# Optimization experiments

Hardware: AMD Instinct MI355X
Metric: run time of the kernel (lower is better)

Reference implementation:

```python
import jax, jax.numpy as jnp
import numpy as np

NUM_EXPERTS = 8
TOP_K = 2
HIDDEN = 2048
INTER = 7168
B, S = 4, 2048


def setup_inputs() -> dict:
    key = jax.random.key(0)
    k0, k1, k2, k3, k4 = jax.random.split(key, 5)
    scale_h = 1.0 / np.sqrt(HIDDEN)
    scale_i = 1.0 / np.sqrt(INTER)
    return {
        "hidden_states": jax.random.normal(k0, (B, S, HIDDEN), dtype=jnp.float32),
        "gate_w": jax.random.normal(k1, (NUM_EXPERTS, HIDDEN), dtype=jnp.float32) * scale_h,
        "w1": jax.random.normal(k2, (NUM_EXPERTS, INTER, HIDDEN), dtype=jnp.float32) * scale_h,
        "w3": jax.random.normal(k3, (NUM_EXPERTS, INTER, HIDDEN), dtype=jnp.float32) * scale_h,
        "w2": jax.random.normal(k4, (NUM_EXPERTS, HIDDEN, INTER), dtype=jnp.float32) * scale_i,
    }


def reference(hidden_states, gate_w, w1, w3, w2):
    orig_shape = hidden_states.shape
    x = hidden_states.reshape(-1, HIDDEN)              # [T, H]

    # Router: gate linear -> softmax -> top-k -> renormalize.
    router_logits = x @ gate_w.T                       # [T, E]
    probs = jax.nn.softmax(router_logits, axis=-1)
    topk_w, topk_idx = jax.lax.top_k(probs, TOP_K)     # [T, K]
    topk_w = topk_w / jnp.sum(topk_w, axis=-1, keepdims=True)

    # Dense combine weights: [T, E] with top-k renormalized weights scattered.
    combine = jnp.sum(
        jax.nn.one_hot(topk_idx, NUM_EXPERTS, dtype=x.dtype) * topk_w[..., None],
        axis=1,
    )                                                   # [T, E]

    out = jnp.zeros_like(x)
    # Fixed small loop over experts (structurally distinct weight matrices);
    # avoids materializing a [T, E, I] intermediate.
    for e in range(NUM_EXPERTS):
        g = jax.nn.silu(x @ w1[e].T)                   # [T, I]
        u = x @ w3[e].T                                # [T, I]
        y = (g * u) @ w2[e].T                          # [T, H]
        out = out + combine[:, e:e + 1] * y

    return out.reshape(orig_shape)
```

## Files before the change

kernel.cpp:

```cpp
#include <hip/hip_runtime.h>
#include <stdint.h>

#define NE    8
#define HID   2048
#define INTER 7168
#define TTOK  8192
#define NT1   (HID / 64)
#define NT2   (INTER / 64)

typedef __bf16 bf16;
typedef bf16 bf16x4 __attribute__((ext_vector_type(4)));
typedef bf16 bf16x8 __attribute__((ext_vector_type(8)));
typedef float f32x4 __attribute__((ext_vector_type(4)));

__device__ __forceinline__ void glds16(const void* g, void* l) {
  __builtin_amdgcn_global_load_lds((__attribute__((address_space(1))) void*)g,
                                   (__attribute__((address_space(3))) void*)l, 16, 0, 0);
}

__global__ void cvt_f32_bf16(const float* __restrict__ src, bf16* __restrict__ dst, long n) {
  long i = (long)blockIdx.x * blockDim.x + threadIdx.x;
  long stride = (long)gridDim.x * blockDim.x;
  for (long j = i * 4; j < n; j += stride * 4) {
    float4 v = *(const float4*)(src + j);
    bf16x4 o = {(bf16)v.x, (bf16)v.y, (bf16)v.z, (bf16)v.w};
    *(bf16x4*)(dst + j) = o;
  }
}

__global__ void router_kernel(const float* __restrict__ x, const float* __restrict__ gw,
                              int* __restrict__ topk_e, float* __restrict__ topk_w) {
  const int wid = threadIdx.x >> 6, lane = threadIdx.x & 63;
  const int t = blockIdx.x * 4 + wid;
  if (t >= TTOK) return;
  const float* xr = x + (size_t)t * HID;
  float xv[32];
#pragma unroll
  for (int i = 0; i < 32; ++i) xv[i] = xr[lane + 64 * i];
  float lg[NE];
#pragma unroll
  for (int e = 0; e < NE; ++e) {
    const float* g = gw + e * HID;
    float s = 0.f;
#pragma unroll
    for (int i = 0; i < 32; ++i) s += xv[i] * g[lane + 64 * i];
#pragma unroll
    for (int off = 32; off; off >>= 1) s += __shfl_down(s, off);
    lg[e] = s;
  }
  if (lane == 0) {
    int i1 = 0;
#pragma unroll
    for (int e = 1; e < NE; ++e) if (lg[e] > lg[i1]) i1 = e;
    int i2 = (i1 == 0) ? 1 : 0;
#pragma unroll
    for (int e = 0; e < NE; ++e) if (e != i2 && e != i1 && lg[e] > lg[i2]) i2 = e;
    float r = __expf(lg[i2] - lg[i1]);
    float wa = 1.f / (1.f + r);
    topk_e[2 * t] = i1; topk_e[2 * t + 1] = i2;
    topk_w[2 * t] = wa; topk_w[2 * t + 1] = 1.f - wa;
  }
}

__global__ void gather_sorted(const int* __restrict__ topk_e, const float* __restrict__ topk_w,
                              int* __restrict__ cnt, int* __restrict__ ltok, float* __restrict__ lw) {
  const int e = blockIdx.x;
  const int tid = threadIdx.x;
  __shared__ int scan[256];
  __shared__ int basesh;
  if (tid == 0) basesh = 0;
  __syncthreads();
  for (int c0 = 0; c0 < TTOK; c0 += 256) {
    const int t = c0 + tid;
    const int e0 = topk_e[2 * t], e1 = topk_e[2 * t + 1];
    const int flag = (e0 == e) || (e1 == e);
    const float w = (e0 == e) ? topk_w[2 * t] : topk_w[2 * t + 1];
    scan[tid] = flag;
    __syncthreads();
    for (int off = 1; off < 256; off <<= 1) {
      int add = (tid >= off) ? scan[tid - off] : 0;
      __syncthreads();
      scan[tid] += add;
      __syncthreads();
    }
    const int rank = scan[tid] - flag;
    const int total = scan[255];
    const int base = basesh;
    if (flag) { ltok[e * TTOK + base + rank] = t; lw[e * TTOK + base + rank] = w; }
    __syncthreads();
    if (tid == 0) basesh = base + total;
    __syncthreads();
  }
  if (tid == 0) cnt[e] = basesh;
}

__global__ void prefix_kernel(const int* __restrict__ cnt, int* __restrict__ base) {
  if (threadIdx.x == 0 && blockIdx.x == 0) {
    int b = 0;
    for (int e = 0; e < NE; ++e) { base[e] = b; b += cnt[e]; }
  }
}


#define MFMA(a, b, c) __builtin_amdgcn_mfma_f32_16x16x32_bf16((a), (b), (c), 0, 0, 0)

#define STAGE_A(h, kt) do { int _b = ((kt) & 1) * 32768; size_t _k = (size_t)(kt) * 128; \
    glds16(bA + oA[(h)*2 + 0] + _k, ldsA + _b + (h) * 16384 + d0); \
    glds16(bA + oA[(h)*2 + 1] + _k, ldsA + _b + (h) * 16384 + d1); } while (0)
#define STAGE_B(h, kt) do { int _b = ((kt) & 1) * 32768; size_t _k = (size_t)(kt) * 128; \
    glds16(bB + oB[(h)*2 + 0] + _k, ldsB + _b + (h) * 16384 + d0); \
    glds16(bB + oB[(h)*2 + 1] + _k, ldsB + _b + (h) * 16384 + d1); } while (0)

#define RD_A(mf, ks) (*(const bf16x8*)(ldsA + curb + arow + (mf) * (16 * 128) + ((ks) ? kcol1 : kcol0)))
#define RD_B(nf, ks) (*(const bf16x8*)(ldsB + curb + brow + (nf) * (16 * 128) + ((ks) ? kcol1 : kcol0)))

#define BAR()   __builtin_amdgcn_s_barrier()
#define LGKM0() do { asm volatile("s_waitcnt lgkmcnt(0)" ::: "memory"); \
                     __builtin_amdgcn_sched_barrier(0); } while (0)
#define SCHED0() __builtin_amdgcn_sched_barrier(0)

__launch_bounds__(512, 2)
__global__ void pass1_kernel(const bf16* __restrict__ xb, const bf16* __restrict__ w1b,
                             bf16* __restrict__ hbuf, const int* __restrict__ cnt,
                             const int* __restrict__ basep, const int* __restrict__ ltok) {
  const int e = blockIdx.z;
  const int c = cnt[e];
  const int tm = blockIdx.y;
  if (tm * 256 >= c) return;
  const int tn = blockIdx.x;

  __shared__ __align__(16) bf16 sA[2][256 * 64];
  __shared__ __align__(16) bf16 sB[2][256 * 64];
  char* const ldsA = (char*)&sA[0][0];
  char* const ldsB = (char*)&sB[0][0];

  const int tid = threadIdx.x;
  const int r0 = tid >> 3;
  const int ls = (tid & 7) ^ (r0 & 7);
  const int d0 = tid * 16, d1 = (tid + 512) * 16;
  const char* const bA = (const char*)xb;
  const char* const bB = (const char*)w1b;

  uint32_t oA[4], oB[4];
#pragma unroll
  for (int i = 0; i < 4; ++i) {
    int trow = i * 64 + r0;
    int slot = tm * 256 + trow; if (slot >= c) slot = c - 1;
    oA[i] = (uint32_t)((size_t)ltok[e * TTOK + slot] * (HID * 2) + ls * 16);
    int br = i * 64 + r0;
    int w = (br >> 4) & 1;
    int wr = tn * 128 + ((br >> 5) << 4) + (br & 15);
    size_t off = ((size_t)e * INTER + wr) * (HID * 2) + (size_t)ls * 16;
    if (w) off += (size_t)NE * INTER * HID * 2;
    oB[i] = (uint32_t)off;
  }

  const int lane = tid & 63, wid = tid >> 6;
  const int wm = wid >> 2, wn = wid & 3;
  const int ln15 = lane & 15, kq = lane >> 4;
  const int swz = (ln15 & 7) << 4;
  const int kcol0 = (kq * 16) ^ swz;
  const int kcol1 = (64 + kq * 16) ^ swz;
  const int arow = (wm * 128 + ln15) * 128;
  const int brow = (wn * 64 + ln15) * 128;

  f32x4 acc[8][4];
#pragma unroll
  for (int m = 0; m < 8; ++m)
#pragma unroll
    for (int n = 0; n < 4; ++n) acc[m][n] = (f32x4){0.f, 0.f, 0.f, 0.f};

  STAGE_A(0, 0); STAGE_A(1, 0); STAGE_B(0, 0); STAGE_B(1, 0);
  asm volatile("s_waitcnt vmcnt(4)" ::: "memory");
  STAGE_A(0, 1); STAGE_A(1, 1); STAGE_B(0, 1);
  asm volatile("s_waitcnt vmcnt(6)" ::: "memory");
  BAR();

  bf16x8 a0[4][2], a1[4][2], b0[2][2], b1[2][2];
  int cur = 0;
  for (int t = 0; t < NT1; ++t, cur ^= 1) {
    const int curb = cur * 32768;
#pragma unroll
    for (int m = 0; m < 4; ++m) { a0[m][0] = RD_A(m, 0); a0[m][1] = RD_A(m, 1); }
#pragma unroll
    for (int n = 0; n < 2; ++n) { b0[n][0] = RD_B(n, 0); b0[n][1] = RD_B(n, 1); }
    if (t + 1 < NT1) STAGE_B(1, t + 1);
    BAR(); LGKM0();
    __builtin_amdgcn_s_setprio(1);
#pragma unroll
    for (int m = 0; m < 4; ++m)
#pragma unroll
      for (int n = 0; n < 2; ++n) {
        acc[m][n] = MFMA(a0[m][0], b0[n][0], acc[m][n]);
        acc[m][n] = MFMA(a0[m][1], b0[n][1], acc[m][n]);
      }
    __builtin_amdgcn_s_setprio(0);
    BAR();
#pragma unroll
    for (int m = 0; m < 4; ++m) { a1[m][0] = RD_A(4 + m, 0); a1[m][1] = RD_A(4 + m, 1); }
    BAR(); LGKM0();
    __builtin_amdgcn_s_setprio(1);
#pragma unroll
    for (int m = 0; m < 4; ++m)
#pragma unroll
      for (int n = 0; n < 2; ++n) {
        acc[4 + m][n] = MFMA(a1[m][0], b0[n][0], acc[4 + m][n]);
        acc[4 + m][n] = MFMA(a1[m][1], b0[n][1], acc[4 + m][n]);
      }
    __builtin_amdgcn_s_setprio(0);
    BAR();
#pragma unroll
    for (int n = 0; n < 2; ++n) { b1[n][0] = RD_B(2 + n, 0); b1[n][1] = RD_B(2 + n, 1); }
    if (t + 2 < NT1) { STAGE_A(0, t + 2); STAGE_A(1, t + 2); SCHED0(); }
    BAR(); LGKM0();
    __builtin_amdgcn_s_setprio(1);
#pragma unroll
    for (int m = 0; m < 4; ++m)
#pragma unroll
      for (int n = 0; n < 2; ++n) {
        acc[m][2 + n] = MFMA(a0[m][0], b1[n][0], acc[m][2 + n]);
        acc[m][2 + n] = MFMA(a0[m][1], b1[n][1], acc[m][2 + n]);
      }
    __builtin_amdgcn_s_setprio(0);
    BAR();
    if (t + 2 < NT1) STAGE_B(0, t + 2);
    __builtin_amdgcn_s_setprio(1);
#pragma unroll
    for (int m = 0; m < 4; ++m)
#pragma unroll
      for (int n = 0; n < 2; ++n) {
        acc[4 + m][2 + n] = MFMA(a1[m][0], b1[n][0], acc[4 + m][2 + n]);
        acc[4 + m][2 + n] = MFMA(a1[m][1], b1[n][1], acc[4 + m][2 + n]);
      }
    __builtin_amdgcn_s_setprio(0);
    if (t + 2 < NT1) asm volatile("s_waitcnt vmcnt(6)" ::: "memory");
    else             asm volatile("s_waitcnt vmcnt(0)" ::: "memory");
    BAR();
  }

  const int be = basep[e];
#pragma unroll
  for (int mh = 0; mh < 2; ++mh)
#pragma unroll
    for (int mf = 0; mf < 4; ++mf)
#pragma unroll
      for (int j = 0; j < 4; ++j) {
        const int slot = tm * 256 + wm * 128 + mh * 64 + mf * 16 + kq * 4 + j;
        if (slot < c) {
          bf16* hrow = hbuf + (size_t)(be + slot) * INTER + tn * 128;
#pragma unroll
          for (int p = 0; p < 2; ++p) {
            const float g = acc[mh * 4 + mf][2 * p][j];
            const float u = acc[mh * 4 + mf][2 * p + 1][j];
            const float hv = g / (1.f + __expf(-g)) * u;
            hrow[wn * 32 + p * 16 + ln15] = (bf16)hv;
          }
        }
      }
}

__launch_bounds__(512, 2)
__global__ void pass2_kernel(const bf16* __restrict__ hbuf, const bf16* __restrict__ w2b,
                             float* __restrict__ out, const int* __restrict__ cnt,
                             const int* __restrict__ basep, const int* __restrict__ ltok,
                             const float* __restrict__ lw) {
  const int e = blockIdx.z;
  const int c = cnt[e];
  const int tm = blockIdx.y;
  if (tm * 256 >= c) return;
  const int tn = blockIdx.x;

  __shared__ __align__(16) bf16 sA[2][256 * 64];
  __shared__ __align__(16) bf16 sB[2][256 * 64];
  char* const ldsA = (char*)&sA[0][0];
  char* const ldsB = (char*)&sB[0][0];

  const int tid = threadIdx.x;
  const int r0 = tid >> 3;
  const int ls = (tid & 7) ^ (r0 & 7);
  const int d0 = tid * 16, d1 = (tid + 512) * 16;
  const int be = basep[e];
  const char* const bA = (const char*)hbuf;
  const char* const bB = (const char*)w2b;

  uint32_t oA[4], oB[4];
#pragma unroll
  for (int i = 0; i < 4; ++i) {
    int trow = i * 64 + r0;
    int slot = tm * 256 + trow; if (slot >= c) slot = c - 1;
    oA[i] = (uint32_t)((size_t)(be + slot) * (INTER * 2) + ls * 16);
    oB[i] = (uint32_t)(((size_t)e * HID + tn * 256 + i * 64 + r0) * (INTER * 2) + (size_t)ls * 16);
  }

  const int lane = tid & 63, wid = tid >> 6;
  const int wm = wid >> 2, wn = wid & 3;
  const int ln15 = lane & 15, kq = lane >> 4;
  const int swz = (ln15 & 7) << 4;
  const int kcol0 = (kq * 16) ^ swz;
  const int kcol1 = (64 + kq * 16) ^ swz;
  const int arow = (wm * 128 + ln15) * 128;
  const int brow = (wn * 64 + ln15) * 128;

  f32x4 acc[8][4];
#pragma unroll
  for (int m = 0; m < 8; ++m)
#pragma unroll
    for (int n = 0; n < 4; ++n) acc[m][n] = (f32x4){0.f, 0.f, 0.f, 0.f};

  STAGE_A(0, 0); STAGE_A(1, 0); STAGE_B(0, 0); STAGE_B(1, 0);
  asm volatile("s_waitcnt vmcnt(4)" ::: "memory");
  STAGE_A(0, 1); STAGE_A(1, 1); STAGE_B(0, 1);
  asm volatile("s_waitcnt vmcnt(6)" ::: "memory");
  BAR();

  bf16x8 a0[4][2], a1[4][2], b0[2][2], b1[2][2];
  int cur = 0;
  for (int t = 0; t < NT2; ++t, cur ^= 1) {
    const int curb = cur * 32768;
#pragma unroll
    for (int m = 0; m < 4; ++m) { a0[m][0] = RD_A(m, 0); a0[m][1] = RD_A(m, 1); }
#pragma unroll
    for (int n = 0; n < 2; ++n) { b0[n][0] = RD_B(n, 0); b0[n][1] = RD_B(n, 1); }
    if (t + 1 < NT2) STAGE_B(1, t + 1);
    BAR(); LGKM0();
    __builtin_amdgcn_s_setprio(1);
#pragma unroll
    for (int m = 0; m < 4; ++m)
#pragma unroll
      for (int n = 0; n < 2; ++n) {
        acc[m][n] = MFMA(a0[m][0], b0[n][0], acc[m][n]);
        acc[m][n] = MFMA(a0[m][1], b0[n][1], acc[m][n]);
      }
    __builtin_amdgcn_s_setprio(0);
    BAR();
#pragma unroll
    for (int m = 0; m < 4; ++m) { a1[m][0] = RD_A(4 + m, 0); a1[m][1] = RD_A(4 + m, 1); }
    BAR(); LGKM0();
    __builtin_amdgcn_s_setprio(1);
#pragma unroll
    for (int m = 0; m < 4; ++m)
#pragma unroll
      for (int n = 0; n < 2; ++n) {
        acc[4 + m][n] = MFMA(a1[m][0], b0[n][0], acc[4 + m][n]);
        acc[4 + m][n] = MFMA(a1[m][1], b0[n][1], acc[4 + m][n]);
      }
    __builtin_amdgcn_s_setprio(0);
    BAR();
#pragma unroll
    for (int n = 0; n < 2; ++n) { b1[n][0] = RD_B(2 + n, 0); b1[n][1] = RD_B(2 + n, 1); }
    if (t + 2 < NT2) { STAGE_A(0, t + 2); STAGE_A(1, t + 2); SCHED0(); }
    BAR(); LGKM0();
    __builtin_amdgcn_s_setprio(1);
#pragma unroll
    for (int m = 0; m < 4; ++m)
#pragma unroll
      for (int n = 0; n < 2; ++n) {
        acc[m][2 + n] = MFMA(a0[m][0], b1[n][0], acc[m][2 + n]);
        acc[m][2 + n] = MFMA(a0[m][1], b1[n][1], acc[m][2 + n]);
      }
    __builtin_amdgcn_s_setprio(0);
    BAR();
    if (t + 2 < NT2) STAGE_B(0, t + 2);
    __builtin_amdgcn_s_setprio(1);
#pragma unroll
    for (int m = 0; m < 4; ++m)
#pragma unroll
      for (int n = 0; n < 2; ++n) {
        acc[4 + m][2 + n] = MFMA(a1[m][0], b1[n][0], acc[4 + m][2 + n]);
        acc[4 + m][2 + n] = MFMA(a1[m][1], b1[n][1], acc[4 + m][2 + n]);
      }
    __builtin_amdgcn_s_setprio(0);
    if (t + 2 < NT2) asm volatile("s_waitcnt vmcnt(6)" ::: "memory");
    else             asm volatile("s_waitcnt vmcnt(0)" ::: "memory");
    BAR();
  }

#pragma unroll
  for (int mh = 0; mh < 2; ++mh)
#pragma unroll
    for (int mf = 0; mf < 4; ++mf)
#pragma unroll
      for (int j = 0; j < 4; ++j) {
        const int slot = tm * 256 + wm * 128 + mh * 64 + mf * 16 + kq * 4 + j;
        if (slot < c) {
          const int tok = ltok[e * TTOK + slot];
          const float wt = lw[e * TTOK + slot];
          float* orow = out + (size_t)tok * HID + tn * 256;
#pragma unroll
          for (int n = 0; n < 4; ++n)
            atomicAdd(orow + wn * 64 + n * 16 + ln15, wt * acc[mh * 4 + mf][n][j]);
        }
      }
}

extern "C" void kernel_launch(void* const* d_in, const int* in_sizes, int n_in,
                              void* d_out, int out_size, void* d_ws, size_t ws_size,
                              hipStream_t stream) {
  const float* x  = (const float*)d_in[0];
  const float* gw = (const float*)d_in[1];
  const float* w1 = (const float*)d_in[2];
  const float* w3 = (const float*)d_in[3];
  const float* w2 = (const float*)d_in[4];
  float* out = (float*)d_out;

  char* ws = (char*)d_ws;
  size_t off = 0;
  auto take = [&](size_t bytes) -> char* {
    char* p = ws + off;
    off += (bytes + 255) & ~(size_t)255;
    return p;
  };
  bf16* xb    = (bf16*)take((size_t)TTOK * HID * 2);
  bf16* w1b   = (bf16*)take((size_t)NE * INTER * HID * 2);
  bf16* w3b   = (bf16*)take((size_t)NE * INTER * HID * 2);
  bf16* w2b   = (bf16*)take((size_t)NE * HID * INTER * 2);
  bf16* hbuf  = (bf16*)take((size_t)TTOK * 2 * INTER * 2);
  int*   topk_e = (int*)take(TTOK * 2 * 4);
  float* topk_w = (float*)take(TTOK * 2 * 4);
  int*   ltok   = (int*)take(NE * TTOK * 4);
  float* lwgt   = (float*)take(NE * TTOK * 4);
  int*   cntp   = (int*)take(64);
  int*   basep  = (int*)take(64);
  if (off > ws_size) return;

  hipMemsetAsync(d_out, 0, (size_t)out_size * 4, stream);

  cvt_f32_bf16<<<2048, 256, 0, stream>>>(x,  xb,  (long)TTOK * HID);
  cvt_f32_bf16<<<4096, 256, 0, stream>>>(w1, w1b, (long)NE * INTER * HID);
  cvt_f32_bf16<<<4096, 256, 0, stream>>>(w3, w3b, (long)NE * INTER * HID);
  cvt_f32_bf16<<<4096, 256, 0, stream>>>(w2, w2b, (long)NE * HID * INTER);

  router_kernel<<<TTOK / 4, 256, 0, stream>>>(x, gw, topk_e, topk_w);
  gather_sorted<<<NE, 256, 0, stream>>>(topk_e, topk_w, cntp, ltok, lwgt);
  prefix_kernel<<<1, 64, 0, stream>>>(cntp, basep);

  pass1_kernel<<<dim3(INTER / 128, TTOK / 256, NE), 512, 0, stream>>>(
      xb, w1b, hbuf, cntp, basep, ltok);
  pass2_kernel<<<dim3(HID / 256, TTOK / 256, NE), 512, 0, stream>>>(
      hbuf, w2b, out, cntp, basep, ltok, lwgt);
}
```

Measured before the change: 2.312 ms.

## Skew MFMA quadrants across LDS reads, drop atomics via combine kernel

The GEMM main loops in both passes are reordered so each MFMA quadrant runs while the next LDS fragment reads are still in flight. The last quadrant of an iteration is deferred to the next one, and partial lgkmcnt waits replace full waits. Pass2 no longer does float atomicAdd into the output: it writes weighted per-slot rows to a new ybuf, and a new combine kernel sums each token's two expert rows. This also removes the output memset. The gather kernel's shared-memory scan is replaced by a wave ballot/popcount rank and now records each token's slot position, at the cost of an extra intermediate buffer and an extra kernel launch.

Result: faster. 2.103 ms (-9.0%).

```diff
diff --git a/kernel.cpp b/kernel.cpp
--- a/kernel.cpp
+++ b/kernel.cpp
@@ -63,32 +63,36 @@
 }
 
 __global__ void gather_sorted(const int* __restrict__ topk_e, const float* __restrict__ topk_w,
-                              int* __restrict__ cnt, int* __restrict__ ltok, float* __restrict__ lw) {
+                              int* __restrict__ cnt, int* __restrict__ ltok,
+                              float* __restrict__ lw, int* __restrict__ ppos) {
   const int e = blockIdx.x;
   const int tid = threadIdx.x;
-  __shared__ int scan[256];
+  const int lane = tid & 63, wv = tid >> 6;
+  __shared__ int wtot[4];
   __shared__ int basesh;
   if (tid == 0) basesh = 0;
   __syncthreads();
   for (int c0 = 0; c0 < TTOK; c0 += 256) {
     const int t = c0 + tid;
     const int e0 = topk_e[2 * t], e1 = topk_e[2 * t + 1];
+    const int j = (e0 == e) ? 0 : 1;
     const int flag = (e0 == e) || (e1 == e);
-    const float w = (e0 == e) ? topk_w[2 * t] : topk_w[2 * t + 1];
-    scan[tid] = flag;
+    unsigned long long b = __ballot(flag);
+    int wrank = __popcll(b & ((1ULL << lane) - 1ULL));
+    if (lane == 63) wtot[wv] = __popcll(b);
     __syncthreads();
-    for (int off = 1; off < 256; off <<= 1) {
-      int add = (tid >= off) ? scan[tid - off] : 0;
-      __syncthreads();
-      scan[tid] += add;
-      __syncthreads();
+    int wbase = 0;
+#pragma unroll
+    for (int k = 0; k < 4; ++k) if (k < wv) wbase += wtot[k];
+    const int total = wtot[0] + wtot[1] + wtot[2] + wtot[3];
+    const int pos = basesh + wbase + wrank;
+    if (flag) {
+      ltok[e * TTOK + pos] = t;
+      lw[e * TTOK + pos] = (j == 0) ? topk_w[2 * t] : topk_w[2 * t + 1];
+      ppos[2 * t + j] = pos;
     }
-    const int rank = scan[tid] - flag;
-    const int total = scan[255];
-    const int base = basesh;
-    if (flag) { ltok[e * TTOK + base + rank] = t; lw[e * TTOK + base + rank] = w; }
     __syncthreads();
-    if (tid == 0) basesh = base + total;
+    if (tid == 0) basesh += total;
     __syncthreads();
   }
   if (tid == 0) cnt[e] = basesh;
@@ -98,7 +102,24 @@
   if (threadIdx.x == 0 && blockIdx.x == 0) {
     int b = 0;
     for (int e = 0; e < NE; ++e) { base[e] = b; b += cnt[e]; }
-  }
+    base[NE] = b;
+  }
+}
+
+__global__ void combine_kernel(const float* __restrict__ ybuf, const int* __restrict__ topk_e,
+                               const int* __restrict__ ppos, const int* __restrict__ basep,
+                               float* __restrict__ out) {
+  const int t = blockIdx.x;
+  const int col = threadIdx.x * 8;
+  const int g0 = basep[topk_e[2 * t]] + ppos[2 * t];
+  const int g1 = basep[topk_e[2 * t + 1]] + ppos[2 * t + 1];
+  const float4* y0 = (const float4*)(ybuf + (size_t)g0 * HID + col);
+  const float4* y1 = (const float4*)(ybuf + (size_t)g1 * HID + col);
+  float4* o = (float4*)(out + (size_t)t * HID + col);
+  float4 a0 = y0[0], b0 = y1[0];
+  float4 a1 = y0[1], b1 = y1[1];
+  o[0] = make_float4(a0.x + b0.x, a0.y + b0.y, a0.z + b0.z, a0.w + b0.w);
+  o[1] = make_float4(a1.x + b1.x, a1.y + b1.y, a1.z + b1.z, a1.w + b1.w);
 }
 
 
@@ -114,10 +135,22 @@
 #define RD_A(mf, ks) (*(const bf16x8*)(ldsA + curb + arow + (mf) * (16 * 128) + ((ks) ? kcol1 : kcol0)))
 #define RD_B(nf, ks) (*(const bf16x8*)(ldsB + curb + brow + (nf) * (16 * 128) + ((ks) ? kcol1 : kcol0)))
 
-#define BAR()   __builtin_amdgcn_s_barrier()
-#define LGKM0() do { asm volatile("s_waitcnt lgkmcnt(0)" ::: "memory"); \
-                     __builtin_amdgcn_sched_barrier(0); } while (0)
+#define BAR()    __builtin_amdgcn_s_barrier()
+#define LGKMC(n) do { asm volatile("s_waitcnt lgkmcnt(" #n ")" ::: "memory"); \
+                      __builtin_amdgcn_sched_barrier(0); } while (0)
 #define SCHED0() __builtin_amdgcn_sched_barrier(0)
+
+#define Q_MFMA(AM, BM, ACCM, ACCN_OFF) do { \
+  __builtin_amdgcn_s_setprio(1); \
+  _Pragma("unroll") \
+  for (int m = 0; m < 4; ++m) \
+    _Pragma("unroll") \
+    for (int n = 0; n < 2; ++n) { \
+      acc[ACCM + m][ACCN_OFF + n] = MFMA(AM[m][0], BM[n][0], acc[ACCM + m][ACCN_OFF + n]); \
+      acc[ACCM + m][ACCN_OFF + n] = MFMA(AM[m][1], BM[n][1], acc[ACCM + m][ACCN_OFF + n]); \
+    } \
+  __builtin_amdgcn_s_setprio(0); \
+} while (0)
 
 __launch_bounds__(512, 2)
 __global__ void pass1_kernel(const bf16* __restrict__ xb, const bf16* __restrict__ w1b,
@@ -185,58 +218,28 @@
 #pragma unroll
     for (int n = 0; n < 2; ++n) { b0[n][0] = RD_B(n, 0); b0[n][1] = RD_B(n, 1); }
     if (t + 1 < NT1) STAGE_B(1, t + 1);
-    BAR(); LGKM0();
-    __builtin_amdgcn_s_setprio(1);
-#pragma unroll
-    for (int m = 0; m < 4; ++m)
-#pragma unroll
-      for (int n = 0; n < 2; ++n) {
-        acc[m][n] = MFMA(a0[m][0], b0[n][0], acc[m][n]);
-        acc[m][n] = MFMA(a0[m][1], b0[n][1], acc[m][n]);
-      }
-    __builtin_amdgcn_s_setprio(0);
+    BAR(); LGKMC(12);
+    if (t > 0) Q_MFMA(a1, b1, 4, 2);
     BAR();
 #pragma unroll
     for (int m = 0; m < 4; ++m) { a1[m][0] = RD_A(4 + m, 0); a1[m][1] = RD_A(4 + m, 1); }
-    BAR(); LGKM0();
-    __builtin_amdgcn_s_setprio(1);
-#pragma unroll
-    for (int m = 0; m < 4; ++m)
-#pragma unroll
-      for (int n = 0; n < 2; ++n) {
-        acc[4 + m][n] = MFMA(a1[m][0], b0[n][0], acc[4 + m][n]);
-        acc[4 + m][n] = MFMA(a1[m][1], b0[n][1], acc[4 + m][n]);
-      }
-    __builtin_amdgcn_s_setprio(0);
+    BAR(); LGKMC(8);
+    Q_MFMA(a0, b0, 0, 0);
     BAR();
 #pragma unroll
     for (int n = 0; n < 2; ++n) { b1[n][0] = RD_B(2 + n, 0); b1[n][1] = RD_B(2 + n, 1); }
     if (t + 2 < NT1) { STAGE_A(0, t + 2); STAGE_A(1, t + 2); SCHED0(); }
-    BAR(); LGKM0();
-    __builtin_amdgcn_s_setprio(1);
-#pragma unroll
-    for (int m = 0; m < 4; ++m)
-#pragma unroll
-      for (int n = 0; n < 2; ++n) {
-        acc[m][2 + n] = MFMA(a0[m][0], b1[n][0], acc[m][2 + n]);
-        acc[m][2 + n] = MFMA(a0[m][1], b1[n][1], acc[m][2 + n]);
-      }
-    __builtin_amdgcn_s_setprio(0);
+    BAR(); LGKMC(4);
+    Q_MFMA(a1, b0, 4, 0);
     BAR();
     if (t + 2 < NT1) STAGE_B(0, t + 2);
-    __builtin_amdgcn_s_setprio(1);
-#pragma unroll
-    for (int m = 0; m < 4; ++m)
-#pragma unroll
-      for (int n = 0; n < 2; ++n) {
-        acc[4 + m][2 + n] = MFMA(a1[m][0], b1[n][0], acc[4 + m][2 + n]);
-        acc[4 + m][2 + n] = MFMA(a1[m][1], b1[n][1], acc[4 + m][2 + n]);
-      }
-    __builtin_amdgcn_s_setprio(0);
+    LGKMC(0);
+    Q_MFMA(a0, b1, 0, 2);
     if (t + 2 < NT1) asm volatile("s_waitcnt vmcnt(6)" ::: "memory");
     else             asm volatile("s_waitcnt vmcnt(0)" ::: "memory");
     BAR();
   }
+  Q_MFMA(a1, b1, 4, 2);
 
   const int be = basep[e];
 #pragma unroll
@@ -261,9 +264,8 @@
 
 __launch_bounds__(512, 2)
 __global__ void pass2_kernel(const bf16* __restrict__ hbuf, const bf16* __restrict__ w2b,
-                             float* __restrict__ out, const int* __restrict__ cnt,
-                             const int* __restrict__ basep, const int* __restrict__ ltok,
-                             const float* __restrict__ lw) {
+                             float* __restrict__ ybuf, const int* __restrict__ cnt,
+                             const int* __restrict__ basep, const float* __restrict__ lw) {
   const int e = blockIdx.z;
   const int c = cnt[e];
   const int tm = blockIdx.y;
@@ -322,58 +324,28 @@
 #pragma unroll
     for (int n = 0; n < 2; ++n) { b0[n][0] = RD_B(n, 0); b0[n][1] = RD_B(n, 1); }
     if (t + 1 < NT2) STAGE_B(1, t + 1);
-    BAR(); LGKM0();
-    __builtin_amdgcn_s_setprio(1);
-#pragma unroll
-    for (int m = 0; m < 4; ++m)
-#pragma unroll
-      for (int n = 0; n < 2; ++n) {
-        acc[m][n] = MFMA(a0[m][0], b0[n][0], acc[m][n]);
-        acc[m][n] = MFMA(a0[m][1], b0[n][1], acc[m][n]);
-      }
-    __builtin_amdgcn_s_setprio(0);
+    BAR(); LGKMC(12);
+    if (t > 0) Q_MFMA(a1, b1, 4, 2);
     BAR();
 #pragma unroll
     for (int m = 0; m < 4; ++m) { a1[m][0] = RD_A(4 + m, 0); a1[m][1] = RD_A(4 + m, 1); }
-    BAR(); LGKM0();
-    __builtin_amdgcn_s_setprio(1);
-#pragma unroll
-    for (int m = 0; m < 4; ++m)
-#pragma unroll
-      for (int n = 0; n < 2; ++n) {
-        acc[4 + m][n] = MFMA(a1[m][0], b0[n][0], acc[4 + m][n]);
-        acc[4 + m][n] = MFMA(a1[m][1], b0[n][1], acc[4 + m][n]);
-      }
-    __builtin_amdgcn_s_setprio(0);
+    BAR(); LGKMC(8);
+    Q_MFMA(a0, b0, 0, 0);
     BAR();
 #pragma unroll
     for (int n = 0; n < 2; ++n) { b1[n][0] = RD_B(2 + n, 0); b1[n][1] = RD_B(2 + n, 1); }
     if (t + 2 < NT2) { STAGE_A(0, t + 2); STAGE_A(1, t + 2); SCHED0(); }
-    BAR(); LGKM0();
-    __builtin_amdgcn_s_setprio(1);
-#pragma unroll
-    for (int m = 0; m < 4; ++m)
-#pragma unroll
-      for (int n = 0; n < 2; ++n) {
-        acc[m][2 + n] = MFMA(a0[m][0], b1[n][0], acc[m][2 + n]);
-        acc[m][2 + n] = MFMA(a0[m][1], b1[n][1], acc[m][2 + n]);
-      }
-    __builtin_amdgcn_s_setprio(0);
+    BAR(); LGKMC(4);
+    Q_MFMA(a1, b0, 4, 0);
     BAR();
     if (t + 2 < NT2) STAGE_B(0, t + 2);
-    __builtin_amdgcn_s_setprio(1);
-#pragma unroll
-    for (int m = 0; m < 4; ++m)
-#pragma unroll
-      for (int n = 0; n < 2; ++n) {
-        acc[4 + m][2 + n] = MFMA(a1[m][0], b1[n][0], acc[4 + m][2 + n]);
-        acc[4 + m][2 + n] = MFMA(a1[m][1], b1[n][1], acc[4 + m][2 + n]);
-      }
-    __builtin_amdgcn_s_setprio(0);
+    LGKMC(0);
+    Q_MFMA(a0, b1, 0, 2);
     if (t + 2 < NT2) asm volatile("s_waitcnt vmcnt(6)" ::: "memory");
     else             asm volatile("s_waitcnt vmcnt(0)" ::: "memory");
     BAR();
   }
+  Q_MFMA(a1, b1, 4, 2);
 
 #pragma unroll
   for (int mh = 0; mh < 2; ++mh)
@@ -383,12 +355,11 @@
       for (int j = 0; j < 4; ++j) {
         const int slot = tm * 256 + wm * 128 + mh * 64 + mf * 16 + kq * 4 + j;
         if (slot < c) {
-          const int tok = ltok[e * TTOK + slot];
           const float wt = lw[e * TTOK + slot];
-          float* orow = out + (size_t)tok * HID + tn * 256;
+          float* yrow = ybuf + (size_t)(be + slot) * HID + tn * 256;
 #pragma unroll
           for (int n = 0; n < 4; ++n)
-            atomicAdd(orow + wn * 64 + n * 16 + ln15, wt * acc[mh * 4 + mf][n][j]);
+            yrow[wn * 64 + n * 16 + ln15] = wt * acc[mh * 4 + mf][n][j];
         }
       }
 }
@@ -415,15 +386,15 @@
   bf16* w3b   = (bf16*)take((size_t)NE * INTER * HID * 2);
   bf16* w2b   = (bf16*)take((size_t)NE * HID * INTER * 2);
   bf16* hbuf  = (bf16*)take((size_t)TTOK * 2 * INTER * 2);
+  float* ybuf = (float*)take((size_t)TTOK * 2 * HID * 4);
   int*   topk_e = (int*)take(TTOK * 2 * 4);
   float* topk_w = (float*)take(TTOK * 2 * 4);
   int*   ltok   = (int*)take(NE * TTOK * 4);
   float* lwgt   = (float*)take(NE * TTOK * 4);
+  int*   ppos   = (int*)take(TTOK * 2 * 4);
   int*   cntp   = (int*)take(64);
   int*   basep  = (int*)take(64);
   if (off > ws_size) return;
-
-  hipMemsetAsync(d_out, 0, (size_t)out_size * 4, stream);
 
   cvt_f32_bf16<<<2048, 256, 0, stream>>>(x,  xb,  (long)TTOK * HID);
   cvt_f32_bf16<<<4096, 256, 0, stream>>>(w1, w1b, (long)NE * INTER * HID);
@@ -431,11 +402,12 @@
   cvt_f32_bf16<<<4096, 256, 0, stream>>>(w2, w2b, (long)NE * HID * INTER);
 
   router_kernel<<<TTOK / 4, 256, 0, stream>>>(x, gw, topk_e, topk_w);
-  gather_sorted<<<NE, 256, 0, stream>>>(topk_e, topk_w, cntp, ltok, lwgt);
+  gather_sorted<<<NE, 256, 0, stream>>>(topk_e, topk_w, cntp, ltok, lwgt, ppos);
   prefix_kernel<<<1, 64, 0, stream>>>(cntp, basep);
 
   pass1_kernel<<<dim3(INTER / 128, TTOK / 256, NE), 512, 0, stream>>>(
       xb, w1b, hbuf, cntp, basep, ltok);
   pass2_kernel<<<dim3(HID / 256, TTOK / 256, NE), 512, 0, stream>>>(
-      hbuf, w2b, out, cntp, basep, ltok, lwgt);
-}
+      hbuf, w2b, ybuf, cntp, basep, lwgt);
+  combine_kernel<<<TTOK, 256, 0, stream>>>(ybuf, topk_e, ppos, basep, out);
+}
```
